# Performance work log

Hardware: AMD Instinct MI355X
Metric: run time of the kernel (lower is better)

The kernel has to match this reference:

```python
import jax, jax.numpy as jnp
import numpy as np

# OFDM/MIMO constants from the source module
N = 512        # subcarriers
N_R = 2        # rx antennas
N_T = 2        # tx antennas
M_BITS = 4     # bits per QAM symbol (16-QAM)
CP = 7         # cyclic prefix = IsiDuration - 1
NO = 1e-5
EBNO_DB = 10.0
BATCH = 4096

# unit-average-power 16-QAM: per-axis levels, index = re_idx + 4*im_idx, bits LSB-first
LEV = jnp.asarray(np.array([-3.0, -1.0, 1.0, 3.0], np.float32) / np.sqrt(10.0))
_idx = np.arange(2 ** M_BITS)
CONST = jnp.asarray(((np.array([-3., -1., 1., 3.]) / np.sqrt(10.))[_idx % 4]
                     + 1j * (np.array([-3., -1., 1., 3.]) / np.sqrt(10.))[_idx // 4]).astype(np.complex64))


def setup_inputs() -> dict:
    key = jax.random.key(0)
    k1, k2, k3 = jax.random.split(key, 3)
    y_data_nld = jax.random.normal(k1, (BATCH, N_R, N + CP, 2), jnp.float32)
    y_ls = jax.random.normal(k2, (BATCH, N_R, N + CP, 2), jnp.float32)
    x_ls_idx = jax.random.randint(k3, (BATCH, N_T, N), 0, 2 ** M_BITS)
    return {"y_data_nld": y_data_nld, "y_ls": y_ls, "x_ls_idx": x_ls_idx}


def _c(x):
    return jax.lax.complex(x[..., 0], x[..., 1])


def _interp_c(xq, xp, fp):
    # fp: [M, P] complex -> [M, N] complex, linear interp per row (np.interp semantics)
    return jax.vmap(lambda fr, fi: jnp.interp(xq, xp, fr) + 1j * jnp.interp(xq, xp, fi))(fp.real, fp.imag)


def _forward(y_data_nld, y_ls, x_ls_idx):
    B = y_data_nld.shape[0]
    pi = 10.0 ** (EBNO_DB / 10.0) * NO * N          # = 0.0512
    sqrt_pi = jnp.sqrt(jnp.float32(pi))

    # strip CP, FFT, normalize (1/N * fft)
    Y = jnp.fft.fft(_c(y_data_nld)[..., CP:], axis=-1) / N            # [B, N_r, N]
    Y_l = jnp.fft.fft(_c(y_ls)[..., CP:], axis=-1) / (N * sqrt_pi)     # [B, N_r, N]

    x_ls = CONST[x_ls_idx]                                             # [B, N_t, N] pilots

    # comb-type LS estimates + linear interpolation to all N subcarriers
    xq = jnp.arange(N, dtype=jnp.float32)
    H_t = []
    for t in range(N_T):
        comb = jnp.arange(t, N, N_T)                                   # pilot subcarriers for tx t
        pil = Y_l[:, :, comb] / x_ls[:, None, t, comb]                 # [B, N_r, N/N_t]
        if t == 0:
            xp = jnp.concatenate([comb, jnp.array([N - 1])]).astype(jnp.float32)
            fp = jnp.concatenate([pil, pil[..., -1:]], axis=-1)
        else:
            xp = jnp.concatenate([jnp.array([0]), comb]).astype(jnp.float32)
            fp = jnp.concatenate([pil[..., :1], pil], axis=-1)
        P = fp.shape[-1]
        H_t.append(_interp_c(xq, xp, fp.reshape(B * N_R, P)).reshape(B, N_R, N))
    Hm = jnp.stack(H_t, axis=-1)                                       # [B, N_r, N, N_t]
    Hm = jnp.transpose(Hm, (0, 2, 1, 3))                               # [B, N, N_r, N_t]

    # per-subcarrier 2x2 linear solve: X_hat = H^{-1} Y / sqrt(pi)
    X_hat = jnp.linalg.solve(Hm, jnp.transpose(Y, (0, 2, 1))[..., None])[..., 0] / sqrt_pi  # [B, N, N_t]
    x_hat_ri = jnp.stack([X_hat.real, X_hat.imag], axis=-1)            # [B, N, N_t, 2]

    # nearest-QAM demap (square 16-QAM: per-axis argmin == joint argmin), bits LSB-first
    vre = jnp.argmin((X_hat.real[..., None] - LEV) ** 2, axis=-1)      # [B, N, N_t]
    vim = jnp.argmin((X_hat.imag[..., None] - LEV) ** 2, axis=-1)
    qidx = vre + 4 * vim
    bits = (qidx[..., None] >> jnp.arange(M_BITS)) & 1                 # [B, N, N_t, m]
    b_hat = jnp.transpose(bits, (0, 2, 1, 3)).reshape(B, N_T, N * M_BITS).astype(jnp.float32)
    return x_hat_ri, b_hat


def reference(y_data_nld, y_ls, x_ls_idx):
    return _forward(y_data_nld, y_ls, x_ls_idx)
```

## Files before the change

### kernel.cpp

```cpp
#include <hip/hip_runtime.h>
#include <math.h>

namespace {

constexpr int NSC  = 512;
constexpr int CP   = 7;
constexpr int NTOT = 519;

__device__ __forceinline__ int padidx(int x) { return x + (x >> 5); }

struct cf { float x, y; };
__device__ __forceinline__ cf cadd(cf a, cf b) { return {a.x + b.x, a.y + b.y}; }
__device__ __forceinline__ cf csub(cf a, cf b) { return {a.x - b.x, a.y - b.y}; }
__device__ __forceinline__ cf cmul(cf a, cf b) { return {a.x*b.x - a.y*b.y, a.x*b.y + a.y*b.x}; }
__device__ __forceinline__ cf mni(cf a) { return {a.y, -a.x}; }

__device__ __forceinline__ void fft8(cf a[8]) {
    const float s = 0.70710678118654752f;
    cf b0 = a[0], b1 = a[4], b2 = a[2], b3 = a[6];
    cf b4 = a[1], b5 = a[5], b6 = a[3], b7 = a[7];
    cf c0 = cadd(b0, b1), c1 = csub(b0, b1);
    cf c2 = cadd(b2, b3), c3 = csub(b2, b3);
    cf c4 = cadd(b4, b5), c5 = csub(b4, b5);
    cf c6 = cadd(b6, b7), c7 = csub(b6, b7);
    cf d0 = cadd(c0, c2), d2 = csub(c0, c2);
    cf d1 = cadd(c1, mni(c3)), d3 = csub(c1, mni(c3));
    cf d4 = cadd(c4, c6), d6 = csub(c4, c6);
    cf d5 = cadd(c5, mni(c7)), d7 = csub(c5, mni(c7));
    cf e5 = { s * (d5.x + d5.y), s * (d5.y - d5.x) };
    cf e6 = mni(d6);
    cf e7 = { s * (d7.y - d7.x), -s * (d7.x + d7.y) };
    a[0] = cadd(d0, d4); a[4] = csub(d0, d4);
    a[1] = cadd(d1, e5); a[5] = csub(d1, e5);
    a[2] = cadd(d2, e6); a[6] = csub(d2, e6);
    a[3] = cadd(d3, e7); a[7] = csub(d3, e7);
}

struct cd { double x, y; };
__device__ __forceinline__ cd cmuld(cd a, cd b) { return {a.x*b.x - a.y*b.y, a.x*b.y + a.y*b.x}; }
__device__ __forceinline__ cd csubd(cd a, cd b) { return {a.x - b.x, a.y - b.y}; }
__device__ __forceinline__ cd cdivd(cd a, cd b) {
    double d = b.x*b.x + b.y*b.y;
    return {(a.x*b.x + a.y*b.y) / d, (a.y*b.x - a.x*b.y) / d};
}

__global__ __launch_bounds__(256, 8) void ofdm_mimo_kernel(
    const float* __restrict__ y_data,
    const float* __restrict__ y_ls,
    const int*   __restrict__ x_idx,
    float*       __restrict__ out,
    int B)
{
    __shared__ float sr[4][528];
    __shared__ float si[4][528];

    const int b   = blockIdx.x;
    const int tid = threadIdx.x;
    const int q   = tid >> 6;
    const int t   = tid & 63;

    const float sc = (float)(1.0 / (512.0 * 0.22627416997969522));

    const int r = q & 1;
    const float* srcp = (q < 2) ? y_data : y_ls;
    const float2* xin = (const float2*)(srcp + ((size_t)(b * 2 + r) * NTOT + CP) * 2);

    cf a[8];
    #pragma unroll
    for (int n2 = 0; n2 < 8; ++n2) {
        float2 v = xin[t + 64 * n2];
        a[n2] = { v.x * sc, v.y * sc };
    }
    fft8(a);

    {
        const int n1 = t >> 3;
        const float w64 = -6.2831853071795864769f / 64.0f;
        #pragma unroll
        for (int k0 = 1; k0 < 8; ++k0) {
            float sn, cs;
            __sincosf(w64 * (float)(n1 * k0), &sn, &cs);
            a[k0] = cmul(a[k0], {cs, sn});
        }
    }
    #pragma unroll
    for (int k0 = 0; k0 < 8; ++k0) {
        int p = padidx(t * 8 + k0);
        sr[q][p] = a[k0].x;
        si[q][p] = a[k0].y;
    }
    __builtin_amdgcn_wave_barrier();

    #pragma unroll
    for (int n1 = 0; n1 < 8; ++n1) {
        int p = padidx(n1 * 64 + (t & 7) * 8 + (t >> 3));
        a[n1] = { sr[q][p], si[q][p] };
    }
    __builtin_amdgcn_wave_barrier();
    fft8(a);

    {
        const int n0 = t & 7, k0 = t >> 3;
        const float w512 = -6.2831853071795864769f / 512.0f;
        #pragma unroll
        for (int k1 = 0; k1 < 8; ++k1) {
            float sn, cs;
            __sincosf(w512 * (float)(n0 * (k0 + 8 * k1)), &sn, &cs);
            a[k1] = cmul(a[k1], {cs, sn});
        }
    }
    #pragma unroll
    for (int k1 = 0; k1 < 8; ++k1) {
        int p = padidx((t & 7) * 64 + (t >> 3) * 8 + k1);
        sr[q][p] = a[k1].x;
        si[q][p] = a[k1].y;
    }
    __builtin_amdgcn_wave_barrier();

    #pragma unroll
    for (int n0 = 0; n0 < 8; ++n0) {
        int p = padidx(n0 * 64 + (t >> 3) * 8 + (t & 7));
        a[n0] = { sr[q][p], si[q][p] };
    }
    __builtin_amdgcn_wave_barrier();
    fft8(a);

    #pragma unroll
    for (int k2 = 0; k2 < 8; ++k2) {
        int p = padidx((t >> 3) + 8 * (t & 7) + 64 * k2);
        sr[q][p] = a[k2].x;
        si[q][p] = a[k2].y;
    }
    __syncthreads();

    const float lev[4] = {-0.9486832980505138f, -0.31622776601683794f,
                           0.31622776601683794f, 0.9486832980505138f};
    float pr[2][2], pim[2][2];
    #pragma unroll
    for (int j = 0; j < 2; ++j) {
        int u  = tid + 256 * j;
        int tt = u >> 8;
        int k  = u & 255;
        int comb = tt + 2 * k;
        int idx = x_idx[((size_t)(b * 2 + tt)) * NSC + comb];
        float xr = lev[idx & 3];
        float xi = lev[(idx >> 2) & 3];
        float inv = 1.0f / (xr * xr + xi * xi);
        int pc = padidx(comb);
        #pragma unroll
        for (int rr = 0; rr < 2; ++rr) {
            float ylr = sr[2 + rr][pc];
            float yli = si[2 + rr][pc];
            pr[j][rr]  = (ylr * xr + yli * xi) * inv;
            pim[j][rr] = (yli * xr - ylr * xi) * inv;
        }
    }
    __syncthreads();
    #pragma unroll
    for (int j = 0; j < 2; ++j) {
        int u  = tid + 256 * j;
        int tt = u >> 8;
        int k  = u & 255;
        #pragma unroll
        for (int rr = 0; rr < 2; ++rr) {
            int p = padidx(rr * 256 + k);
            sr[2 + tt][p] = pr[j][rr];
            si[2 + tt][p] = pim[j][rr];
        }
    }
    __syncthreads();

    #pragma unroll
    for (int ni = 0; ni < 2; ++ni) {
        const int n = tid + 256 * ni;
        cd H[2][2];
        #pragma unroll
        for (int rr = 0; rr < 2; ++rr) {
            float2 h0, h1;
            if ((n & 1) == 0) {
                int p = padidx(rr * 256 + (n >> 1));
                h0 = make_float2(sr[2][p], si[2][p]);
            } else if (n == NSC - 1) {
                int p = padidx(rr * 256 + 255);
                h0 = make_float2(sr[2][p], si[2][p]);
            } else {
                int pa = padidx(rr * 256 + (n >> 1));
                int pb = padidx(rr * 256 + (n >> 1) + 1);
                h0 = make_float2(0.5f * (sr[2][pa] + sr[2][pb]),
                                 0.5f * (si[2][pa] + si[2][pb]));
            }
            if (n & 1) {
                int p = padidx(rr * 256 + (n >> 1));
                h1 = make_float2(sr[3][p], si[3][p]);
            } else if (n == 0) {
                int p = padidx(rr * 256 + 0);
                h1 = make_float2(sr[3][p], si[3][p]);
            } else {
                int pa = padidx(rr * 256 + (n >> 1) - 1);
                int pb = padidx(rr * 256 + (n >> 1));
                h1 = make_float2(0.5f * (sr[3][pa] + sr[3][pb]),
                                 0.5f * (si[3][pa] + si[3][pb]));
            }
            H[rr][0] = {(double)h0.x, (double)h0.y};
            H[rr][1] = {(double)h1.x, (double)h1.y};
        }
        int pn = padidx(n);
        cd Y0 = {(double)sr[0][pn], (double)si[0][pn]};
        cd Y1 = {(double)sr[1][pn], (double)si[1][pn]};

        cd det = csubd(cmuld(H[0][0], H[1][1]), cmuld(H[0][1], H[1][0]));
        cd X0  = cdivd(csubd(cmuld(H[1][1], Y0), cmuld(H[0][1], Y1)), det);
        cd X1  = cdivd(csubd(cmuld(H[0][0], Y1), cmuld(H[1][0], Y0)), det);

        float4* xo = (float4*)(out + (size_t)b * 2048 + (size_t)n * 4);
        *xo = make_float4((float)X0.x, (float)X0.y, (float)X1.x, (float)X1.y);

        const double bnd = 0.6324555320336759;
        auto qi = [&](double v) -> int {
            return (v <= -bnd) ? 0 : (v <= 0.0) ? 1 : (v <= bnd) ? 2 : 3;
        };
        int vre0 = qi(X0.x), vim0 = qi(X0.y);
        int vre1 = qi(X1.x), vim1 = qi(X1.y);

        size_t bbase = (size_t)B * 2048;
        float4* b0 = (float4*)(out + bbase + ((size_t)b * 2 + 0) * 2048 + (size_t)n * 4);
        *b0 = make_float4((float)(vre0 & 1), (float)((vre0 >> 1) & 1),
                          (float)(vim0 & 1), (float)((vim0 >> 1) & 1));
        float4* b1 = (float4*)(out + bbase + ((size_t)b * 2 + 1) * 2048 + (size_t)n * 4);
        *b1 = make_float4((float)(vre1 & 1), (float)((vre1 >> 1) & 1),
                          (float)(vim1 & 1), (float)((vim1 >> 1) & 1));
    }
}

}

extern "C" void kernel_launch(void* const* d_in, const int* in_sizes, int n_in,
                              void* d_out, int out_size, void* d_ws, size_t ws_size,
                              hipStream_t stream) {
    const float* y_data = (const float*)d_in[0];
    const float* y_ls   = (const float*)d_in[1];
    const int*   x_idx  = (const int*)d_in[2];
    float* out = (float*)d_out;

    int B = in_sizes[0] / (2 * NTOT * 2);
    ofdm_mimo_kernel<<<B, 256, 0, stream>>>(y_data, y_ls, x_idx, out, B);
}
```

Measured before the change: 39.32 us.

## Interleave LDS complex storage, use recurrence twiddles, branchless interp, shared reciprocal

```diff
diff --git a/kernel.cpp b/kernel.cpp
--- a/kernel.cpp
+++ b/kernel.cpp
@@ -1,5 +1,4 @@
 #include <hip/hip_runtime.h>
-#include <math.h>
 
 namespace {
 
@@ -7,7 +6,7 @@
 constexpr int CP   = 7;
 constexpr int NTOT = 519;
 
-__device__ __forceinline__ int padidx(int x) { return x + (x >> 5); }
+__device__ __forceinline__ int p2(int x) { return x + (x >> 4); }
 
 struct cf { float x, y; };
 __device__ __forceinline__ cf cadd(cf a, cf b) { return {a.x + b.x, a.y + b.y}; }
@@ -39,10 +38,6 @@
 struct cd { double x, y; };
 __device__ __forceinline__ cd cmuld(cd a, cd b) { return {a.x*b.x - a.y*b.y, a.x*b.y + a.y*b.x}; }
 __device__ __forceinline__ cd csubd(cd a, cd b) { return {a.x - b.x, a.y - b.y}; }
-__device__ __forceinline__ cd cdivd(cd a, cd b) {
-    double d = b.x*b.x + b.y*b.y;
-    return {(a.x*b.x + a.y*b.y) / d, (a.y*b.x - a.x*b.y) / d};
-}
 
 __global__ __launch_bounds__(256, 8) void ofdm_mimo_kernel(
     const float* __restrict__ y_data,
@@ -51,8 +46,7 @@
     float*       __restrict__ out,
     int B)
 {
-    __shared__ float sr[4][528];
-    __shared__ float si[4][528];
+    __shared__ cf sb[4][544];
 
     const int b   = blockIdx.x;
     const int tid = threadIdx.x;
@@ -61,6 +55,9 @@
 
     const float sc = (float)(1.0 / (512.0 * 0.22627416997969522));
 
+    const float W64A  = -6.2831853071795864769f / 64.0f;
+    const float W512A = -6.2831853071795864769f / 512.0f;
+
     const int r = q & 1;
     const float* srcp = (q < 2) ? y_data : y_ls;
     const float2* xin = (const float2*)(srcp + ((size_t)(b * 2 + r) * NTOT + CP) * 2);
@@ -75,67 +72,56 @@
 
     {
         const int n1 = t >> 3;
-        const float w64 = -6.2831853071795864769f / 64.0f;
+        float sn, cs;
+        __sincosf(W64A * (float)n1, &sn, &cs);
+        cf w1 = {cs, sn}, w = w1;
         #pragma unroll
         for (int k0 = 1; k0 < 8; ++k0) {
-            float sn, cs;
-            __sincosf(w64 * (float)(n1 * k0), &sn, &cs);
-            a[k0] = cmul(a[k0], {cs, sn});
-        }
-    }
-    #pragma unroll
-    for (int k0 = 0; k0 < 8; ++k0) {
-        int p = padidx(t * 8 + k0);
-        sr[q][p] = a[k0].x;
-        si[q][p] = a[k0].y;
-    }
-    __builtin_amdgcn_wave_barrier();
-
-    #pragma unroll
-    for (int n1 = 0; n1 < 8; ++n1) {
-        int p = padidx(n1 * 64 + (t & 7) * 8 + (t >> 3));
-        a[n1] = { sr[q][p], si[q][p] };
-    }
+            a[k0] = cmul(a[k0], w);
+            w = cmul(w, w1);
+        }
+    }
+    #pragma unroll
+    for (int k0 = 0; k0 < 8; ++k0) sb[q][p2(t * 8 + k0)] = a[k0];
+    __builtin_amdgcn_wave_barrier();
+
+    #pragma unroll
+    for (int n1 = 0; n1 < 8; ++n1)
+        a[n1] = sb[q][p2(n1 * 64 + (t & 7) * 8 + (t >> 3))];
     __builtin_amdgcn_wave_barrier();
     fft8(a);
 
     {
         const int n0 = t & 7, k0 = t >> 3;
-        const float w512 = -6.2831853071795864769f / 512.0f;
+        float sn, cs, sn2, cs2;
+        __sincosf(W512A * (float)(n0 * k0), &sn, &cs);
+        __sincosf(W64A * (float)n0, &sn2, &cs2);
+        cf w = {cs, sn}, st = {cs2, sn2};
         #pragma unroll
         for (int k1 = 0; k1 < 8; ++k1) {
-            float sn, cs;
-            __sincosf(w512 * (float)(n0 * (k0 + 8 * k1)), &sn, &cs);
-            a[k1] = cmul(a[k1], {cs, sn});
-        }
-    }
-    #pragma unroll
-    for (int k1 = 0; k1 < 8; ++k1) {
-        int p = padidx((t & 7) * 64 + (t >> 3) * 8 + k1);
-        sr[q][p] = a[k1].x;
-        si[q][p] = a[k1].y;
-    }
-    __builtin_amdgcn_wave_barrier();
-
-    #pragma unroll
-    for (int n0 = 0; n0 < 8; ++n0) {
-        int p = padidx(n0 * 64 + (t >> 3) * 8 + (t & 7));
-        a[n0] = { sr[q][p], si[q][p] };
-    }
+            a[k1] = cmul(a[k1], w);
+            w = cmul(w, st);
+        }
+    }
+    #pragma unroll
+    for (int k1 = 0; k1 < 8; ++k1)
+        sb[q][p2((t & 7) * 64 + (t >> 3) * 8 + k1)] = a[k1];
+    __builtin_amdgcn_wave_barrier();
+
+    #pragma unroll
+    for (int n0 = 0; n0 < 8; ++n0)
+        a[n0] = sb[q][p2(n0 * 64 + (t >> 3) * 8 + (t & 7))];
     __builtin_amdgcn_wave_barrier();
     fft8(a);
 
     #pragma unroll
-    for (int k2 = 0; k2 < 8; ++k2) {
-        int p = padidx((t >> 3) + 8 * (t & 7) + 64 * k2);
-        sr[q][p] = a[k2].x;
-        si[q][p] = a[k2].y;
-    }
+    for (int k2 = 0; k2 < 8; ++k2)
+        sb[q][p2((t >> 3) + 8 * (t & 7) + 64 * k2)] = a[k2];
     __syncthreads();
 
     const float lev[4] = {-0.9486832980505138f, -0.31622776601683794f,
                            0.31622776601683794f, 0.9486832980505138f};
-    float pr[2][2], pim[2][2];
+    cf pv[2][2];
     #pragma unroll
     for (int j = 0; j < 2; ++j) {
         int u  = tid + 256 * j;
@@ -146,13 +132,11 @@
         float xr = lev[idx & 3];
         float xi = lev[(idx >> 2) & 3];
         float inv = 1.0f / (xr * xr + xi * xi);
-        int pc = padidx(comb);
         #pragma unroll
         for (int rr = 0; rr < 2; ++rr) {
-            float ylr = sr[2 + rr][pc];
-            float yli = si[2 + rr][pc];
-            pr[j][rr]  = (ylr * xr + yli * xi) * inv;
-            pim[j][rr] = (yli * xr - ylr * xi) * inv;
+            cf yl = sb[2 + rr][p2(comb)];
+            pv[j][rr] = { (yl.x * xr + yl.y * xi) * inv,
+                          (yl.y * xr - yl.x * xi) * inv };
         }
     }
     __syncthreads();
@@ -162,55 +146,44 @@
         int tt = u >> 8;
         int k  = u & 255;
         #pragma unroll
-        for (int rr = 0; rr < 2; ++rr) {
-            int p = padidx(rr * 256 + k);
-            sr[2 + tt][p] = pr[j][rr];
-            si[2 + tt][p] = pim[j][rr];
-        }
+        for (int rr = 0; rr < 2; ++rr)
+            sb[2 + tt][p2(rr * 256 + k)] = pv[j][rr];
     }
     __syncthreads();
 
     #pragma unroll
     for (int ni = 0; ni < 2; ++ni) {
         const int n = tid + 256 * ni;
+        const int kp = n >> 1;
+        const int kR = (kp + 1 < 256) ? kp + 1 : 255;
+        const int kL = (kp - 1 > 0) ? kp - 1 : 0;
+        const float wA = (n & 1) ? 0.5f : 0.0f;
+        const float wB = (n & 1) ? 0.0f : 0.5f;
+
         cd H[2][2];
         #pragma unroll
         for (int rr = 0; rr < 2; ++rr) {
-            float2 h0, h1;
-            if ((n & 1) == 0) {
-                int p = padidx(rr * 256 + (n >> 1));
-                h0 = make_float2(sr[2][p], si[2][p]);
-            } else if (n == NSC - 1) {
-                int p = padidx(rr * 256 + 255);
-                h0 = make_float2(sr[2][p], si[2][p]);
-            } else {
-                int pa = padidx(rr * 256 + (n >> 1));
-                int pb = padidx(rr * 256 + (n >> 1) + 1);
-                h0 = make_float2(0.5f * (sr[2][pa] + sr[2][pb]),
-                                 0.5f * (si[2][pa] + si[2][pb]));
-            }
-            if (n & 1) {
-                int p = padidx(rr * 256 + (n >> 1));
-                h1 = make_float2(sr[3][p], si[3][p]);
-            } else if (n == 0) {
-                int p = padidx(rr * 256 + 0);
-                h1 = make_float2(sr[3][p], si[3][p]);
-            } else {
-                int pa = padidx(rr * 256 + (n >> 1) - 1);
-                int pb = padidx(rr * 256 + (n >> 1));
-                h1 = make_float2(0.5f * (sr[3][pa] + sr[3][pb]),
-                                 0.5f * (si[3][pa] + si[3][pb]));
-            }
+            cf L0 = sb[2][p2(rr * 256 + kp)];
+            cf R0 = sb[2][p2(rr * 256 + kR)];
+            cf h0 = { L0.x + wA * (R0.x - L0.x), L0.y + wA * (R0.y - L0.y) };
+            cf R1 = sb[3][p2(rr * 256 + kp)];
+            cf L1 = sb[3][p2(rr * 256 + kL)];
+            cf h1 = { R1.x + wB * (L1.x - R1.x), R1.y + wB * (L1.y - R1.y) };
             H[rr][0] = {(double)h0.x, (double)h0.y};
             H[rr][1] = {(double)h1.x, (double)h1.y};
         }
-        int pn = padidx(n);
-        cd Y0 = {(double)sr[0][pn], (double)si[0][pn]};
-        cd Y1 = {(double)sr[1][pn], (double)si[1][pn]};
-
-        cd det = csubd(cmuld(H[0][0], H[1][1]), cmuld(H[0][1], H[1][0]));
-        cd X0  = cdivd(csubd(cmuld(H[1][1], Y0), cmuld(H[0][1], Y1)), det);
-        cd X1  = cdivd(csubd(cmuld(H[0][0], Y1), cmuld(H[1][0], Y0)), det);
+        cf y0 = sb[0][p2(n)], y1 = sb[1][p2(n)];
+        cd Y0 = {(double)y0.x, (double)y0.y};
+        cd Y1 = {(double)y1.x, (double)y1.y};
+
+        cd det  = csubd(cmuld(H[0][0], H[1][1]), cmuld(H[0][1], H[1][0]));
+        cd num0 = csubd(cmuld(H[1][1], Y0), cmuld(H[0][1], Y1));
+        cd num1 = csubd(cmuld(H[0][0], Y1), cmuld(H[1][0], Y0));
+        double invden = 1.0 / (det.x * det.x + det.y * det.y);
+        cd X0 = { (num0.x * det.x + num0.y * det.y) * invden,
+                  (num0.y * det.x - num0.x * det.y) * invden };
+        cd X1 = { (num1.x * det.x + num1.y * det.y) * invden,
+                  (num1.y * det.x - num1.x * det.y) * invden };
 
         float4* xo = (float4*)(out + (size_t)b * 2048 + (size_t)n * 4);
         *xo = make_float4((float)X0.x, (float)X0.y, (float)X1.x, (float)X1.y);
```

After: 35.27 us. -10.3%, faster.
